# Kernel tuning notes

Measured on AMD Instinct MI355X. Metric: run time of the kernel, lower is better.

Reference implementation:

```python
import jax, jax.numpy as jnp
import numpy as np

Hh, Ww, Cc = 8, 8, 16        # observation grid h, w, channels
N = Hh * Ww                  # 64 graph nodes (one per grid cell)
B = 4096                     # batch
HEADS, COUT = 4, 32          # GAT heads, per-head output dim (concat -> 128)
HID, ADIM = 128, 6           # hidden_dim, action_dim
GAT_OUT = N * HEADS * COUT   # 8192 flattened GAT output per sample
NEG = -9e15


def _grid_adj():
    # 4-connected grid graph with self loops (make_graph's static edge structure)
    A = np.zeros((N, N), np.int32)
    for r in range(Hh):
        for c in range(Ww):
            i = r * Ww + c
            A[i, i] = 1
            for dr, dc in ((1, 0), (-1, 0), (0, 1), (0, -1)):
                rr, cc = r + dr, c + dc
                if 0 <= rr < Hh and 0 <= cc < Ww:
                    A[i, rr * Ww + cc] = 1
    return jnp.asarray(A)


def setup_inputs() -> dict:
    key = jax.random.key(0)
    ks = iter(jax.random.split(key, 40))
    p = lambda *s: jax.random.normal(next(ks), s, jnp.float32) * 0.1
    z = lambda *s: jnp.zeros(s, jnp.float32)
    return dict(
        x=jax.random.normal(next(ks), (B, Hh * Ww * Cc), jnp.float32),
        adj=_grid_adj(),
        actor_h=z(B, HID), actor_c=z(B, HID),
        critic_h=z(B, HID), critic_c=z(B, HID),
        gat1_W=p(Cc, HEADS * COUT), gat1_b=z(HEADS * COUT), gat1_a=p(HEADS, 2 * COUT),
        d1_W=p(GAT_OUT, HID), d1_b=z(HID),
        lstm1_Wi=p(HID, 4 * HID), lstm1_Wh=p(HID, 4 * HID), lstm1_b=z(4 * HID),
        ln1_s=jnp.ones((HID,), jnp.float32), ln1_bi=z(HID),
        d2_W=p(HID, HID), d2_b=z(HID),
        d3_W=p(HID, HID), d3_b=z(HID),
        dout_W=p(HID, ADIM), dout_b=z(ADIM),
        gat2_W=p(Cc, HEADS * COUT), gat2_b=z(HEADS * COUT), gat2_a=p(HEADS, 2 * COUT),
        c1_W=p(GAT_OUT, HID), c1_b=z(HID),
        lstm2_Wi=p(HID, 4 * HID), lstm2_Wh=p(HID, 4 * HID), lstm2_b=z(4 * HID),
        ln2_s=jnp.ones((HID,), jnp.float32), ln2_bi=z(HID),
        c2_W=p(HID, HID), c2_b=z(HID),
        c3_W=p(HID, HID), c3_b=z(HID),
        cout_W=p(HID, 1), cout_b=z(1),
    )


def _gat(feats, adj, W, b, a):
    # feats: [B,N,Cc]; adj: [N,N] int; multi-head GAT with concat heads
    h = (feats @ W + b).reshape(B, N, HEADS, COUT)           # [B,N,H,C]
    ls = jnp.einsum('bnhc,hc->bnh', h, a[:, :COUT])          # source logit
    ld = jnp.einsum('bnhc,hc->bnh', h, a[:, COUT:])          # dest logit
    logits = jax.nn.leaky_relu(ls[:, :, None, :] + ld[:, None, :, :], 0.2)  # [B,N,N,H]
    logits = jnp.where(adj[None, :, :, None] > 0, logits, NEG)
    attn = jax.nn.softmax(logits, axis=2)                    # over neighbors
    return jnp.einsum('bnmh,bmhc->bnhc', attn, h).reshape(B, -1)  # [B, N*H*C]


def _lstm(h, c, xin, Wi, Wh, bh):
    # flax OptimizedLSTMCell: gates in order i,f,g,o; bias only on hidden path
    z = xin @ Wi + h @ Wh + bh
    i, f, g, o = jnp.split(z, 4, axis=-1)
    nc = jax.nn.sigmoid(f) * c + jax.nn.sigmoid(i) * jnp.tanh(g)
    nh = jax.nn.sigmoid(o) * jnp.tanh(nc)
    return nh, nc


def _ln(v, s, b):
    mu = v.mean(-1, keepdims=True)
    var = v.var(-1, keepdims=True)
    return (v - mu) * jax.lax.rsqrt(var + 1e-6) * s + b


def reference(x, adj, actor_h, actor_c, critic_h, critic_c,
              gat1_W, gat1_b, gat1_a, d1_W, d1_b,
              lstm1_Wi, lstm1_Wh, lstm1_b, ln1_s, ln1_bi,
              d2_W, d2_b, d3_W, d3_b, dout_W, dout_b,
              gat2_W, gat2_b, gat2_a, c1_W, c1_b,
              lstm2_Wi, lstm2_Wh, lstm2_b, ln2_s, ln2_bi,
              c2_W, c2_b, c3_W, c3_b, cout_W, cout_b):
    act = jnp.tanh
    feats = x.reshape(B, N, Cc)
    # actor branch
    am = act(_gat(feats, adj, gat1_W, gat1_b, gat1_a) @ d1_W + d1_b)
    a_h, a_c = _lstm(actor_h, actor_c, am, lstm1_Wi, lstm1_Wh, lstm1_b)
    am = _ln(a_h, ln1_s, ln1_bi)
    am = act(am @ d2_W + d2_b)
    am = act(am @ d3_W + d3_b)
    logits = am @ dout_W + dout_b                            # Categorical logits
    # critic branch
    cm = act(_gat(feats, adj, gat2_W, gat2_b, gat2_a) @ c1_W + c1_b)
    c_h, c_c = _lstm(critic_h, critic_c, cm, lstm2_Wi, lstm2_Wh, lstm2_b)
    cm = _ln(c_h, ln2_s, ln2_bi)
    cm = act(cm @ c2_W + c2_b)
    cm = act(cm @ c3_W + c3_b)
    value = (cm @ cout_W + cout_b).squeeze(-1)
    return logits, value, a_h, a_c, c_h, c_c
```

## Files before the change

kernel.cpp:

```cpp
#include <hip/hip_runtime.h>
#include <hip/hip_bf16.h>

#define BATCH 4096
#define NN    64
#define CIN   16
#define NHEAD 4
#define CO    32
#define HC    128
#define HID   128
#define ADIM  6
#define K1    8192
#define LDH   136
#define KSPLIT 8

typedef __attribute__((ext_vector_type(8))) short bf16x8;
typedef __attribute__((ext_vector_type(8))) unsigned short u16x8;
typedef __attribute__((ext_vector_type(4))) float f32x4;

__device__ __forceinline__ float bf2f(unsigned short u) {
    unsigned int v = ((unsigned int)u) << 16;
    return __uint_as_float(v);
}
__device__ __forceinline__ unsigned short f2bf(float x) {
    union { __hip_bfloat16 h; unsigned short u; } cv;
    cv.h = __float2bfloat16(x);
    return cv.u;
}
__device__ __forceinline__ float sigmf(float x) { return 1.f / (1.f + expf(-x)); }

__device__ __forceinline__ void gload_lds16(const void* g, void* l) {
    __builtin_amdgcn_global_load_lds(
        (const __attribute__((address_space(1))) unsigned int*)(uintptr_t)g,
        (__attribute__((address_space(3))) unsigned int*)(uintptr_t)l,
        16, 0, 0);
}

struct TJob { const float* in; unsigned short* out; int K; int N; int ldo; };
struct TJobs { TJob j[8]; };

__global__ __launch_bounds__(256) void k_prep(
    const float* __restrict__ d1W, const float* __restrict__ c1W,
    unsigned short* __restrict__ Wt1, unsigned short* __restrict__ Wt2,
    TJobs jobs,
    const float* __restrict__ ha, const float* __restrict__ hc,
    unsigned short* __restrict__ X,
    const int* __restrict__ adj, unsigned long long* __restrict__ masks,
    const float* __restrict__ l1b, const float* __restrict__ l2b,
    const float* __restrict__ b2,  const float* __restrict__ c2b,
    const float* __restrict__ b3,  const float* __restrict__ c3b,
    float* __restrict__ biasz, float* __restrict__ b2p, float* __restrict__ b3p,
    const float* __restrict__ g1W, const float* __restrict__ g2W,
    const float* __restrict__ g1a, const float* __restrict__ g2a,
    const float* __restrict__ g1b, const float* __restrict__ g2b,
    unsigned short* __restrict__ wtg,
    float* __restrict__ blsld)
{
    const int bid = blockIdx.x;
    const int t   = threadIdx.x;

    if (bid < 1024) {
        __shared__ float s[64][33];
        const int  zsel = bid >> 9;
        const float* W  = zsel ? c1W : d1W;
        unsigned short* Wt = zsel ? Wt2 : Wt1;
        const int k0 = (bid & 127) * 64;
        const int n0 = ((bid >> 7) & 3) * 32;
        const int kr = t >> 5, nc = t & 31;
#pragma unroll
        for (int i = 0; i < 8; ++i)
            s[kr + 8 * i][nc] = W[(size_t)(k0 + kr + 8 * i) * HC + n0 + nc];
        __syncthreads();
#pragma unroll
        for (int j = 0; j < 8; ++j) {
            const int idx = j * 256 + t;
            const int n = idx >> 6, k = idx & 63;
            Wt[(size_t)(n0 + n) * K1 + k0 + k] = f2bf(s[k][n]);
        }
    } else if (bid < 1536) {
        const int b   = bid - 1024;
        const int job = b >> 6, idx = b & 63;
        const TJob jb = jobs.j[job];
        const int ntk = jb.K >> 5, ntn = jb.N >> 5;
        if (idx >= ntk * ntn) return;
        const int tk = idx % ntk, tn = idx / ntk;
        __shared__ float s2[32][33];
        const int kr = t >> 5, nc = t & 31;
        const int k0 = tk * 32, n0 = tn * 32;
#pragma unroll
        for (int i = 0; i < 4; ++i)
            s2[kr + 8 * i][nc] = jb.in[(size_t)(k0 + kr + 8 * i) * jb.N + n0 + nc];
        __syncthreads();
#pragma unroll
        for (int i = 0; i < 4; ++i) {
            const int idx2 = i * 256 + t;
            const int n = idx2 >> 5, k = idx2 & 31;
            jb.out[(size_t)(n0 + n) * jb.ldo + k0 + k] = f2bf(s2[k][n]);
        }
    } else if (bid < 2560) {
        const int gid = (bid - 1536) * 256 + t;
        const int zi  = gid >> 17;
        const int rem = gid & 131071;
        const int s3  = rem >> 5, c4 = rem & 31;
        const float4 v = reinterpret_cast<const float4*>(zi ? hc : ha)[(size_t)s3 * 32 + c4];
        ushort4 u;
        u.x = f2bf(v.x); u.y = f2bf(v.y); u.z = f2bf(v.z); u.w = f2bf(v.w);
        reinterpret_cast<ushort4*>(X + (size_t)zi * BATCH * 256 + (size_t)s3 * 256 + 128)[c4] = u;
    } else {
#pragma unroll
        for (int it = 0; it < 4; ++it) {
            const int tt = t + it * 256;
            if (tt < NN) {
                unsigned long long m = 0ull;
                for (int j = 0; j < NN; ++j)
                    if (adj[tt * NN + j] > 0) m |= (1ull << j);
                masks[tt] = m;
            }
            biasz[tt] = (tt < 512) ? l1b[tt] : l2b[tt - 512];
            if (tt < HID) {
                b2p[tt]       = b2[tt];
                b2p[HID + tt] = c2b[tt];
                b3p[tt]       = b3[tt];
                b3p[HID + tt] = c3b[tt];
            }
        }
#pragma unroll
        for (int q = 0; q < 16; ++q) {
            const int idx = t * 16 + q;
            const int set = idx >> 11;
            const int rem = idx & 2047;
            const int col = rem >> 4, k = rem & 15;
            wtg[set * 2304 + col * 16 + k] = f2bf((set ? g2W : g1W)[k * HC + col]);
        }
        {
            const int set = t >> 7, rem = t & 127;
            const int e = rem >> 4, k = rem & 15;
            const float* W  = set ? g2W : g1W;
            const float* aa = set ? g2a : g1a;
            const int hdh = e & 3, off = (e < 4) ? 0 : 32;
            float v = 0.f;
            for (int c = 0; c < 32; ++c)
                v += W[k * HC + hdh * 32 + c] * aa[hdh * 64 + off + c];
            wtg[set * 2304 + (128 + e) * 16 + k] = f2bf(v);
            wtg[set * 2304 + (136 + e) * 16 + k] = 0;
        }
        if (t < 16) {
            const int s2 = t >> 3, e2 = t & 7;
            const float* bb2 = s2 ? g2b : g1b;
            const float* aa2 = s2 ? g2a : g1a;
            const int h2 = e2 & 3, o2 = (e2 < 4) ? 0 : 32;
            float bv = 0.f;
            for (int c = 0; c < 32; ++c)
                bv += bb2[h2 * 32 + c] * aa2[h2 * 64 + o2 + c];
            blsld[s2 * 8 + e2] = bv;
        }
    }
}

struct GatW { const unsigned short* Wt; const float* b; const float* bls; unsigned short* out; };
struct GatArgs { GatW g[2]; };

__global__ __launch_bounds__(256) void k_gat(
    const float* __restrict__ x,
    const unsigned long long* __restrict__ masks,
    GatArgs ga, int zbase)
{
    const GatW gw = ga.g[zbase + blockIdx.y];
    const unsigned short* __restrict__ Wtg = gw.Wt;
    const float* __restrict__ bias = gw.b;
    const float* __restrict__ bls  = gw.bls;
    unsigned short* __restrict__ out = gw.out;

    union UB {
        struct { unsigned short feat[64][16]; unsigned short wt[144][16]; } stg;
        unsigned short P[2][64][72];
    };
    __shared__ UB u;
    __shared__ unsigned short s_hT[128][72];
    __shared__ float s_ls[64][4];
    __shared__ float s_ld[64][4];
    __shared__ float s_bias[HC];
    __shared__ float s_bls[8];
    __shared__ unsigned long long s_mask[NN];

    const int t = threadIdx.x;
    const int b = blockIdx.x;

    {
        const int n = t >> 2, c0 = (t & 3) * 4;
        const float4 v = reinterpret_cast<const float4*>(x + (size_t)b * (NN * CIN))[t];
        ushort4 q;
        q.x = f2bf(v.x); q.y = f2bf(v.y); q.z = f2bf(v.z); q.w = f2bf(v.w);
        *reinterpret_cast<ushort4*>(&u.stg.feat[n][c0]) = q;
        if (t < 144) {
            *reinterpret_cast<u16x8*>(&u.stg.wt[t][0]) = *reinterpret_cast<const u16x8*>(Wtg + t * 16);
            *reinterpret_cast<u16x8*>(&u.stg.wt[t][8]) = *reinterpret_cast<const u16x8*>(Wtg + t * 16 + 8);
        }
        if (t < HC) s_bias[t] = bias[t];
        if (t < 8)  s_bls[t] = bls[t];
        if (t < NN) s_mask[t] = masks[t];
    }
    __syncthreads();

    const int w = t >> 6, lane = t & 63;
    const int row16 = lane & 15;
    const int jr4   = lane >> 4;

    {
        const bool lo = lane < 32;
        const int k0 = (jr4 & 1) * 8;
        const bf16x8 zf = { 0, 0, 0, 0, 0, 0, 0, 0 };
        const bf16x8 aF = lo ? *reinterpret_cast<const bf16x8*>(&u.stg.feat[w * 16 + row16][k0]) : zf;
        bf16x8 bF[9];
#pragma unroll
        for (int ct = 0; ct < 9; ++ct)
            bF[ct] = lo ? *reinterpret_cast<const bf16x8*>(&u.stg.wt[ct * 16 + row16][k0]) : zf;
        f32x4 acc[9] = {};
#pragma unroll
        for (int ct = 0; ct < 9; ++ct)
            acc[ct] = __builtin_amdgcn_mfma_f32_16x16x32_bf16(aF, bF[ct], acc[ct], 0, 0, 0);
#pragma unroll
        for (int ct = 0; ct < 8; ++ct) {
            const int col = ct * 16 + row16;
            const float bv = s_bias[col];
            ushort4 q;
            q.x = f2bf(acc[ct][0] + bv);
            q.y = f2bf(acc[ct][1] + bv);
            q.z = f2bf(acc[ct][2] + bv);
            q.w = f2bf(acc[ct][3] + bv);
            *reinterpret_cast<ushort4*>(&s_hT[col][w * 16 + jr4 * 4]) = q;
        }
        if (row16 < 8) {
            const float bb = s_bls[row16];
#pragma unroll
            for (int j = 0; j < 4; ++j) {
                const int r = w * 16 + jr4 * 4 + j;
                if (row16 < 4) s_ls[r][row16]     = acc[8][j] + bb;
                else           s_ld[r][row16 - 4] = acc[8][j] + bb;
            }
        }
    }
    __syncthreads();

    const int n  = t >> 2;
    const int hd = t & 3;
    float p[5]; int mc[5]; bool ok[5];
    {
        const unsigned long long m = s_mask[n];
        const int cand[5] = { n - 8, n - 1, n, n + 1, n + 8 };
#pragma unroll
        for (int e = 0; e < 5; ++e) {
            const int cm = cand[e];
            const bool inr = (cm >= 0) && (cm < NN);
            mc[e] = inr ? cm : n;
            ok[e] = inr && ((m >> mc[e]) & 1ull);
        }
        const float lsn = s_ls[n][hd];
        float sum = 0.f;
#pragma unroll
        for (int e = 0; e < 5; ++e) {
            float v = lsn + s_ld[mc[e]][hd];
            v = (v > 0.f) ? v : 0.2f * v;
            p[e] = ok[e] ? __expf(v) : 0.f;
            sum += p[e];
        }
        const float inv = 1.f / sum;
#pragma unroll
        for (int e = 0; e < 5; ++e) p[e] *= inv;
    }

    {
        char* pb = (char*)&u.P[0][0][0];
#pragma unroll
        for (int i = 0; i < 9; ++i)
            *reinterpret_cast<unsigned long long*>(pb + t * 72 + i * 8) = 0ull;
    }
    __syncthreads();

    unsigned short* ob = out + (size_t)b * K1;

#pragma unroll
    for (int pass = 0; pass < 2; ++pass) {
        if ((hd >> 1) == pass) {
#pragma unroll
            for (int e = 0; e < 5; ++e)
                if (ok[e]) u.P[hd & 1][n][mc[e]] = f2bf(p[e]);
        }
        __syncthreads();

        const int hh  = pass * 2 + (w >> 1);
        const int ph  = w >> 1;
        const int mtb = (w & 1) * 2;
        f32x4 acc[2][2] = {};
#pragma unroll
        for (int kt = 0; kt < 2; ++kt) {
            const int kof = kt * 32 + jr4 * 8;
            bf16x8 aF[2], bF[2];
#pragma unroll
            for (int mtl = 0; mtl < 2; ++mtl)
                aF[mtl] = *reinterpret_cast<const bf16x8*>(&u.P[ph][(mtb + mtl) * 16 + row16][kof]);
#pragma unroll
            for (int nt = 0; nt < 2; ++nt)
                bF[nt] = *reinterpret_cast<const bf16x8*>(&s_hT[hh * 32 + nt * 16 + row16][kof]);
#pragma unroll
            for (int mtl = 0; mtl < 2; ++mtl)
#pragma unroll
                for (int nt = 0; nt < 2; ++nt)
                    acc[mtl][nt] = __builtin_amdgcn_mfma_f32_16x16x32_bf16(
                        aF[mtl], bF[nt], acc[mtl][nt], 0, 0, 0);
        }
#pragma unroll
        for (int mtl = 0; mtl < 2; ++mtl)
#pragma unroll
            for (int nt = 0; nt < 2; ++nt) {
                const int ch = hh * 32 + nt * 16 + row16;
#pragma unroll
                for (int j = 0; j < 4; ++j) {
                    const int node = (mtb + mtl) * 16 + jr4 * 4 + j;
                    ob[node * HC + ch] = f2bf(acc[mtl][nt][j]);
                }
            }
        if (pass == 0) __syncthreads();
    }
}

__global__ __launch_bounds__(256) void k_mmsk(
    const unsigned short* __restrict__ A0, const unsigned short* __restrict__ A1,
    const unsigned short* __restrict__ Bt0, const unsigned short* __restrict__ Bt1,
    float* __restrict__ accum)
{
    __shared__ unsigned short sbuf[2][160 * 64];

    const int br   = blockIdx.y;
    const unsigned short* A  = br ? A1 : A0;
    const unsigned short* Bt = br ? Bt1 : Bt0;
    float* acc_out = accum + (size_t)br * BATCH * HID;

    const int t    = threadIdx.x;
    const int w    = t >> 6;
    const int lane = t & 63;
    const int m0   = blockIdx.x * 32;
    const int kbase = blockIdx.z * (K1 / KSPLIT);
    const int kiters = (K1 / KSPLIT) / 64;

    const char* srcp[5];
    int ldsoff[5];
#pragma unroll
    for (int q = 0; q < 5; ++q) {
        const int c     = w * 5 + q;
        const int p     = c * 1024 + lane * 16;
        const int prow  = p >> 7;
        const int pslot = (p >> 4) & 7;
        const int lslot = pslot ^ (prow & 7);
        ldsoff[q] = c * 1024;
        if (c < 4)
            srcp[q] = (const char*)(A + (size_t)(m0 + prow) * K1 + kbase + lslot * 8);
        else
            srcp[q] = (const char*)(Bt + (size_t)(prow - 32) * K1 + kbase + lslot * 8);
    }

    f32x4 acc[2][2] = {};

#pragma unroll
    for (int q = 0; q < 5; ++q)
        gload_lds16(srcp[q], (char*)&sbuf[0][0] + ldsoff[q]);
    __syncthreads();

    int buf = 0;
    for (int it = 0; it < kiters; ++it) {
        if (it + 1 < kiters) {
            const size_t kbyte = (size_t)(it + 1) * 128;
#pragma unroll
            for (int q = 0; q < 5; ++q)
                gload_lds16(srcp[q] + kbyte, (char*)&sbuf[buf ^ 1][0] + ldsoff[q]);
        }
        const char* bb = (const char*)&sbuf[buf][0];
        bf16x8 aF[2][2], bF[2][2];
#pragma unroll
        for (int kb = 0; kb < 2; ++kb) {
            const int slot = kb * 4 + (lane >> 4);
#pragma unroll
            for (int rb = 0; rb < 2; ++rb) {
                const int row = rb * 16 + (lane & 15);
                aF[rb][kb] = *(const bf16x8*)(bb + row * 128 + ((slot ^ (row & 7)) << 4));
            }
#pragma unroll
            for (int cb = 0; cb < 2; ++cb) {
                const int row = 32 + w * 32 + cb * 16 + (lane & 15);
                bF[cb][kb] = *(const bf16x8*)(bb + row * 128 + ((slot ^ (row & 7)) << 4));
            }
        }
#pragma unroll
        for (int kb = 0; kb < 2; ++kb)
#pragma unroll
            for (int rb = 0; rb < 2; ++rb)
#pragma unroll
                for (int cb = 0; cb < 2; ++cb)
                    acc[rb][cb] = __builtin_amdgcn_mfma_f32_16x16x32_bf16(
                        aF[rb][kb], bF[cb][kb], acc[rb][cb], 0, 0, 0);
        __syncthreads();
        buf ^= 1;
    }

    const int col0 = w * 32;
    const int r0   = (lane >> 4) * 4;
    const int cc   = lane & 15;
#pragma unroll
    for (int rb = 0; rb < 2; ++rb)
#pragma unroll
        for (int cb = 0; cb < 2; ++cb) {
            const int col = col0 + cb * 16 + cc;
#pragma unroll
            for (int j = 0; j < 4; ++j) {
                const int row = m0 + rb * 16 + r0 + j;
                atomicAdd(&acc_out[(size_t)row * HID + col], acc[rb][cb][j]);
            }
        }
}

__global__ __launch_bounds__(256) void k_epi(
    const float* __restrict__ accum,
    const float* __restrict__ biasA, const float* __restrict__ biasB,
    unsigned short* __restrict__ X)
{
    const int zi  = blockIdx.y;
    const int gid = blockIdx.x * 256 + threadIdx.x;
    const int s = gid >> 5, c4 = gid & 31;
    const float* bias = zi ? biasB : biasA;
    const float4 v  = reinterpret_cast<const float4*>(accum + (size_t)zi * BATCH * HID)[gid];
    const float4 bv = reinterpret_cast<const float4*>(bias)[c4];
    ushort4 u;
    u.x = f2bf(tanhf(v.x + bv.x));
    u.y = f2bf(tanhf(v.y + bv.y));
    u.z = f2bf(tanhf(v.z + bv.z));
    u.w = f2bf(tanhf(v.w + bv.w));
    unsigned short* Xo = X + (size_t)zi * BATCH * 256;
    reinterpret_cast<ushort4*>(Xo + (size_t)s * 256)[c4] = u;
}

__global__ __launch_bounds__(256) void k_mm(
    const unsigned short* __restrict__ A, size_t aZ, int lda,
    const unsigned short* __restrict__ Bt, size_t bZ,
    const float* __restrict__ bias, size_t biasZ,
    float* __restrict__ outF, unsigned short* __restrict__ outB,
    size_t oZ, int ldo, int kiters, int act)
{
    __shared__ unsigned short sbuf[2][160 * 64];

    const int t    = threadIdx.x;
    const int w    = t >> 6;
    const int lane = t & 63;
    const int m0   = blockIdx.x * 32;
    const int n0   = blockIdx.y * 128;
    const int z    = blockIdx.z;
    const int K    = kiters * 64;

    const unsigned short* Az = A  + (size_t)z * aZ;
    const unsigned short* Bz = Bt + (size_t)z * bZ + (size_t)n0 * K;

    const char* srcp[5];
    int ldsoff[5];
#pragma unroll
    for (int q = 0; q < 5; ++q) {
        const int c     = w * 5 + q;
        const int p     = c * 1024 + lane * 16;
        const int prow  = p >> 7;
        const int pslot = (p >> 4) & 7;
        const int lslot = pslot ^ (prow & 7);
        ldsoff[q] = c * 1024;
        if (c < 4)
            srcp[q] = (const char*)(Az + (size_t)(m0 + prow) * lda + lslot * 8);
        else
            srcp[q] = (const char*)(Bz + (size_t)(prow - 32) * K + lslot * 8);
    }

    f32x4 acc[2][2] = {};

#pragma unroll
    for (int q = 0; q < 5; ++q)
        gload_lds16(srcp[q], (char*)&sbuf[0][0] + ldsoff[q]);
    __syncthreads();

    int buf = 0;
    for (int it = 0; it < kiters; ++it) {
        if (it + 1 < kiters) {
            const size_t kbyte = (size_t)(it + 1) * 128;
#pragma unroll
            for (int q = 0; q < 5; ++q)
                gload_lds16(srcp[q] + kbyte, (char*)&sbuf[buf ^ 1][0] + ldsoff[q]);
        }
        const char* bb = (const char*)&sbuf[buf][0];
        bf16x8 aF[2][2], bF[2][2];
#pragma unroll
        for (int kb = 0; kb < 2; ++kb) {
            const int slot = kb * 4 + (lane >> 4);
#pragma unroll
            for (int rb = 0; rb < 2; ++rb) {
                const int row = rb * 16 + (lane & 15);
                aF[rb][kb] = *(const bf16x8*)(bb + row * 128 + ((slot ^ (row & 7)) << 4));
            }
#pragma unroll
            for (int cb = 0; cb < 2; ++cb) {
                const int row = 32 + w * 32 + cb * 16 + (lane & 15);
                bF[cb][kb] = *(const bf16x8*)(bb + row * 128 + ((slot ^ (row & 7)) << 4));
            }
        }
#pragma unroll
        for (int kb = 0; kb < 2; ++kb)
#pragma unroll
            for (int rb = 0; rb < 2; ++rb)
#pragma unroll
                for (int cb = 0; cb < 2; ++cb)
                    acc[rb][cb] = __builtin_amdgcn_mfma_f32_16x16x32_bf16(
                        aF[rb][kb], bF[cb][kb], acc[rb][cb], 0, 0, 0);
        __syncthreads();
        buf ^= 1;
    }

    const int col0 = w * 32;
    const int r0   = (lane >> 4) * 4;
    const int cc   = lane & 15;
#pragma unroll
    for (int rb = 0; rb < 2; ++rb)
#pragma unroll
        for (int cb = 0; cb < 2; ++cb) {
            const int col = col0 + cb * 16 + cc;
            const float bv = bias ? bias[(size_t)z * biasZ + n0 + col] : 0.f;
#pragma unroll
            for (int j = 0; j < 4; ++j) {
                const int row = m0 + rb * 16 + r0 + j;
                float v = acc[rb][cb][j] + bv;
                if (act) v = tanhf(v);
                const size_t off = (size_t)z * oZ + (size_t)row * ldo + n0 + col;
                if (outB) outB[off] = f2bf(v);
                else      outF[off] = v;
            }
        }
}

__global__ __launch_bounds__(256) void k_tail(
    const float* __restrict__ zbuf,
    const float* __restrict__ c0a, const float* __restrict__ c0c,
    const float* __restrict__ sA,  const float* __restrict__ bA,
    const float* __restrict__ sC,  const float* __restrict__ bC,
    const unsigned short* __restrict__ W23t,
    const float* __restrict__ b2p, const float* __restrict__ b3p,
    const float* __restrict__ doW, const float* __restrict__ dob,
    const float* __restrict__ coW, const float* __restrict__ cob,
    float* __restrict__ hA, float* __restrict__ cA,
    float* __restrict__ hC, float* __restrict__ cC,
    float* __restrict__ logits, float* __restrict__ value)
{
    __shared__ unsigned short s_ln[32][LDH];
    __shared__ unsigned short s_t2[32][LDH];
    __shared__ unsigned short s_t3[32][LDH];
    __shared__ unsigned short s_w[128][LDH];

    const int t  = threadIdx.x;
    const int zi = blockIdx.y;
    const int s0 = blockIdx.x * 32;

    const unsigned short* W2 = W23t + (size_t)zi * HID * HID;
    const unsigned short* W3 = W23t + (size_t)(2 + zi) * HID * HID;

    {
        const int s  = t >> 3, l8 = t & 7;
        const int gb = s0 + s;
        const float* zr  = zbuf + (size_t)zi * BATCH * 512 + (size_t)gb * 512;
        const float* c0  = (zi ? c0c : c0a) + (size_t)gb * HID;
        float* oh = (zi ? hC : hA) + (size_t)gb * HID;
        float* oc = (zi ? cC : cA) + (size_t)gb * HID;
        const float* lns = zi ? sC : sA;
        const float* lnb = zi ? bC : bA;
        const int u0 = l8 * 16;

        float nh16[16];
        float sum = 0.f, sumsq = 0.f;
#pragma unroll
        for (int r4 = 0; r4 < 4; ++r4) {
            const int u = u0 + r4 * 4;
            const float4 gi = *reinterpret_cast<const float4*>(&zr[u]);
            const float4 gf = *reinterpret_cast<const float4*>(&zr[128 + u]);
            const float4 gg = *reinterpret_cast<const float4*>(&zr[256 + u]);
            const float4 go = *reinterpret_cast<const float4*>(&zr[384 + u]);
            const float4 cv = *reinterpret_cast<const float4*>(&c0[u]);
            float4 ncv, nhv;
            ncv.x = sigmf(gf.x) * cv.x + sigmf(gi.x) * tanhf(gg.x);
            ncv.y = sigmf(gf.y) * cv.y + sigmf(gi.y) * tanhf(gg.y);
            ncv.z = sigmf(gf.z) * cv.z + sigmf(gi.z) * tanhf(gg.z);
            ncv.w = sigmf(gf.w) * cv.w + sigmf(gi.w) * tanhf(gg.w);
            nhv.x = sigmf(go.x) * tanhf(ncv.x);
            nhv.y = sigmf(go.y) * tanhf(ncv.y);
            nhv.z = sigmf(go.z) * tanhf(ncv.z);
            nhv.w = sigmf(go.w) * tanhf(ncv.w);
            *reinterpret_cast<float4*>(&oc[u]) = ncv;
            *reinterpret_cast<float4*>(&oh[u]) = nhv;
            nh16[r4 * 4 + 0] = nhv.x; nh16[r4 * 4 + 1] = nhv.y;
            nh16[r4 * 4 + 2] = nhv.z; nh16[r4 * 4 + 3] = nhv.w;
            sum   += nhv.x + nhv.y + nhv.z + nhv.w;
            sumsq += nhv.x * nhv.x + nhv.y * nhv.y + nhv.z * nhv.z + nhv.w * nhv.w;
        }
        for (int msk = 1; msk < 8; msk <<= 1) {
            sum   += __shfl_xor(sum, msk, 8);
            sumsq += __shfl_xor(sumsq, msk, 8);
        }
        const float mu   = sum * (1.f / 128.f);
        const float var  = sumsq * (1.f / 128.f) - mu * mu;
        const float rstd = rsqrtf(var + 1e-6f);
        u16x8 lo, hi;
#pragma unroll
        for (int r = 0; r < 8; ++r) {
            lo[r] = f2bf((nh16[r] - mu) * rstd * lns[u0 + r] + lnb[u0 + r]);
            hi[r] = f2bf((nh16[8 + r] - mu) * rstd * lns[u0 + 8 + r] + lnb[u0 + 8 + r]);
        }
        *reinterpret_cast<u16x8*>(&s_ln[s][u0])     = lo;
        *reinterpret_cast<u16x8*>(&s_ln[s][u0 + 8]) = hi;

        const int col = t >> 1, half = (t & 1) * 64;
#pragma unroll
        for (int q = 0; q < 8; ++q) {
            const u16x8 wv = *reinterpret_cast<const u16x8*>(W2 + col * HID + half + q * 8);
            *reinterpret_cast<u16x8*>(&s_w[col][half + q * 8]) = wv;
        }
    }
    __syncthreads();

    const int w = t >> 6, lane = t & 63;
    const int row16 = lane & 15, k08 = (lane >> 4) * 8;

    {
        f32x4 acc[2][2] = {};
#pragma unroll
        for (int ks = 0; ks < 4; ++ks) {
            bf16x8 aF[2], bF[2];
#pragma unroll
            for (int rt = 0; rt < 2; ++rt)
                aF[rt] = *reinterpret_cast<const bf16x8*>(&s_ln[rt * 16 + row16][ks * 32 + k08]);
#pragma unroll
            for (int ct = 0; ct < 2; ++ct)
                bF[ct] = *reinterpret_cast<const bf16x8*>(&s_w[w * 32 + ct * 16 + row16][ks * 32 + k08]);
#pragma unroll
            for (int rt = 0; rt < 2; ++rt)
#pragma unroll
                for (int ct = 0; ct < 2; ++ct)
                    acc[rt][ct] = __builtin_amdgcn_mfma_f32_16x16x32_bf16(
                        aF[rt], bF[ct], acc[rt][ct], 0, 0, 0);
        }
#pragma unroll
        for (int rt = 0; rt < 2; ++rt)
#pragma unroll
            for (int ct = 0; ct < 2; ++ct) {
                const int col = w * 32 + ct * 16 + row16;
                const float bv = b2p[zi * HID + col];
#pragma unroll
                for (int j = 0; j < 4; ++j)
                    s_t2[rt * 16 + (lane >> 4) * 4 + j][col] = f2bf(tanhf(acc[rt][ct][j] + bv));
            }
    }
    __syncthreads();

    {
        const int col = t >> 1, half = (t & 1) * 64;
#pragma unroll
        for (int q = 0; q < 8; ++q) {
            const u16x8 wv = *reinterpret_cast<const u16x8*>(W3 + col * HID + half + q * 8);
            *reinterpret_cast<u16x8*>(&s_w[col][half + q * 8]) = wv;
        }
    }
    __syncthreads();

    {
        f32x4 acc[2][2] = {};
#pragma unroll
        for (int ks = 0; ks < 4; ++ks) {
            bf16x8 aF[2], bF[2];
#pragma unroll
            for (int rt = 0; rt < 2; ++rt)
                aF[rt] = *reinterpret_cast<const bf16x8*>(&s_t2[rt * 16 + row16][ks * 32 + k08]);
#pragma unroll
            for (int ct = 0; ct < 2; ++ct)
                bF[ct] = *reinterpret_cast<const bf16x8*>(&s_w[w * 32 + ct * 16 + row16][ks * 32 + k08]);
#pragma unroll
            for (int rt = 0; rt < 2; ++rt)
#pragma unroll
                for (int ct = 0; ct < 2; ++ct)
                    acc[rt][ct] = __builtin_amdgcn_mfma_f32_16x16x32_bf16(
                        aF[rt], bF[ct], acc[rt][ct], 0, 0, 0);
        }
#pragma unroll
        for (int rt = 0; rt < 2; ++rt)
#pragma unroll
            for (int ct = 0; ct < 2; ++ct) {
                const int col = w * 32 + ct * 16 + row16;
                const float bv = b3p[zi * HID + col];
#pragma unroll
                for (int j = 0; j < 4; ++j)
                    s_t3[rt * 16 + (lane >> 4) * 4 + j][col] = f2bf(tanhf(acc[rt][ct][j] + bv));
            }
    }
    __syncthreads();

    if (zi == 0) {
        if (t < 32 * ADIM) {
            const int s = t / ADIM, a2 = t % ADIM;
            float acc = dob[a2];
            for (int k = 0; k < HID; ++k)
                acc = fmaf(bf2f(s_t3[s][k]), doW[k * ADIM + a2], acc);
            logits[(size_t)(s0 + s) * ADIM + a2] = acc;
        }
    } else {
        if (t < 32) {
            float acc = cob[0];
            for (int k = 0; k < HID; ++k)
                acc = fmaf(bf2f(s_t3[t][k]), coW[k], acc);
            value[s0 + t] = acc;
        }
    }
}

extern "C" void kernel_launch(void* const* d_in, const int* in_sizes, int n_in,
                              void* d_out, int out_size, void* d_ws, size_t ws_size,
                              hipStream_t stream)
{
    (void)in_sizes; (void)n_in; (void)out_size;

    const float* x        = (const float*)d_in[0];
    const int*   adj      = (const int*)  d_in[1];
    const float* actor_h  = (const float*)d_in[2];
    const float* actor_c  = (const float*)d_in[3];
    const float* critic_h = (const float*)d_in[4];
    const float* critic_c = (const float*)d_in[5];
    const float* gat1_W   = (const float*)d_in[6];
    const float* gat1_b   = (const float*)d_in[7];
    const float* gat1_a   = (const float*)d_in[8];
    const float* d1_W     = (const float*)d_in[9];
    const float* d1_b     = (const float*)d_in[10];
    const float* l1_Wi    = (const float*)d_in[11];
    const float* l1_Wh    = (const float*)d_in[12];
    const float* l1_b     = (const float*)d_in[13];
    const float* ln1_s    = (const float*)d_in[14];
    const float* ln1_b    = (const float*)d_in[15];
    const float* d2_W     = (const float*)d_in[16];
    const float* d2_b     = (const float*)d_in[17];
    const float* d3_W     = (const float*)d_in[18];
    const float* d3_b     = (const float*)d_in[19];
    const float* dout_W   = (const float*)d_in[20];
    const float* dout_b   = (const float*)d_in[21];
    const float* gat2_W   = (const float*)d_in[22];
    const float* gat2_b   = (const float*)d_in[23];
    const float* gat2_a   = (const float*)d_in[24];
    const float* c1_W     = (const float*)d_in[25];
    const float* c1_b     = (const float*)d_in[26];
    const float* l2_Wi    = (const float*)d_in[27];
    const float* l2_Wh    = (const float*)d_in[28];
    const float* l2_b     = (const float*)d_in[29];
    const float* ln2_s    = (const float*)d_in[30];
    const float* ln2_b    = (const float*)d_in[31];
    const float* c2_W     = (const float*)d_in[32];
    const float* c2_b     = (const float*)d_in[33];
    const float* c3_W     = (const float*)d_in[34];
    const float* c3_b     = (const float*)d_in[35];
    const float* cout_W   = (const float*)d_in[36];
    const float* cout_b   = (const float*)d_in[37];

    float* out      = (float*)d_out;
    float* o_logits = out;
    float* o_value  = out + (size_t)BATCH * ADIM;
    float* o_ah     = o_value + BATCH;
    float* o_ac     = o_ah + (size_t)BATCH * HID;
    float* o_ch     = o_ac + (size_t)BATCH * HID;
    float* o_cc     = o_ch + (size_t)BATCH * HID;

    char* ws = (char*)d_ws;
    const size_t MB = 1024 * 1024;
    const size_t KB = 1024;
    unsigned long long* masks = (unsigned long long*)ws;
    float* bias_z = (float*)(ws + 4 * KB);
    float* b2p    = (float*)(ws + 8 * KB);
    float* b3p    = (float*)(ws + 12 * KB);
    unsigned short* wtg = (unsigned short*)(ws + 16 * KB);
    float* blsld  = (float*)(ws + 60 * KB);
    float* accum  = (float*)(ws + 64 * KB);
    unsigned short* Wt1  = (unsigned short*)(ws + 64 * KB + 4 * MB);
    unsigned short* Wt2  = (unsigned short*)(ws + 64 * KB + 6 * MB);
    unsigned short* Wcat = (unsigned short*)(ws + 64 * KB + 8 * MB);
    unsigned short* W23t = (unsigned short*)(ws + 64 * KB + 8 * MB + 512 * KB);
    unsigned short* X    = (unsigned short*)(ws + 64 * KB + 8 * MB + 768 * KB);
    const size_t off_big = 64 * KB + 8 * MB + 768 * KB + 4 * MB;
    char* big = ws + off_big;
    unsigned short* gatA = (unsigned short*)big;
    const bool dual = ws_size >= off_big + 128 * MB;
    unsigned short* gatB = dual ? (unsigned short*)(big + 64 * MB) : gatA;
    float*          zbuf = (float*)big;

    TJobs tj;
    tj.j[0] = { l1_Wi, Wcat,                        HID, 512, 256 };
    tj.j[1] = { l1_Wh, Wcat + 128,                  HID, 512, 256 };
    tj.j[2] = { l2_Wi, Wcat + 512 * 256,            HID, 512, 256 };
    tj.j[3] = { l2_Wh, Wcat + 512 * 256 + 128,      HID, 512, 256 };
    tj.j[4] = { d2_W,  W23t,                        HID, HID, HID };
    tj.j[5] = { c2_W,  W23t + 128 * 128,            HID, HID, HID };
    tj.j[6] = { d3_W,  W23t + 2 * 128 * 128,        HID, HID, HID };
    tj.j[7] = { c3_W,  W23t + 3 * 128 * 128,        HID, HID, HID };
    hipLaunchKernelGGL(k_prep, dim3(2561), dim3(256), 0, stream,
                       d1_W, c1_W, Wt1, Wt2, tj,
                       actor_h, critic_h, X,
                       adj, masks, l1_b, l2_b, d2_b, c2_b, d3_b, c3_b,
                       bias_z, b2p, b3p, gat1_W, gat2_W,
                       gat1_a, gat2_a, gat1_b, gat2_b, wtg, blsld);

    GatArgs ga;
    ga.g[0] = { wtg,        gat1_b, blsld,     gatA };
    ga.g[1] = { wtg + 2304, gat2_b, blsld + 8, gatB };

    if (dual) {
        hipMemsetAsync(accum, 0, (size_t)2 * BATCH * HID * 4, stream);
        hipLaunchKernelGGL(k_gat, dim3(BATCH, 2), dim3(256), 0, stream,
                           x, masks, ga, 0);
        hipLaunchKernelGGL(k_mmsk, dim3(BATCH / 32, 2, KSPLIT), dim3(256), 0, stream,
                           gatA, gatB, Wt1, Wt2, accum);
        hipLaunchKernelGGL(k_epi, dim3(512, 2), dim3(256), 0, stream,
                           accum, d1_b, c1_b, X);
    } else {
        hipLaunchKernelGGL(k_gat, dim3(BATCH, 1), dim3(256), 0, stream,
                           x, masks, ga, 0);
        hipMemsetAsync(accum, 0, (size_t)BATCH * HID * 4, stream);
        hipLaunchKernelGGL(k_mmsk, dim3(BATCH / 32, 1, KSPLIT), dim3(256), 0, stream,
                           gatA, gatA, Wt1, Wt1, accum);
        hipLaunchKernelGGL(k_epi, dim3(512, 1), dim3(256), 0, stream,
                           accum, d1_b, c1_b, X);
        hipLaunchKernelGGL(k_gat, dim3(BATCH, 1), dim3(256), 0, stream,
                           x, masks, ga, 1);
        hipMemsetAsync(accum, 0, (size_t)BATCH * HID * 4, stream);
        hipLaunchKernelGGL(k_mmsk, dim3(BATCH / 32, 1, KSPLIT), dim3(256), 0, stream,
                           gatA, gatA, Wt2, Wt2, accum);
        hipLaunchKernelGGL(k_epi, dim3(512, 1), dim3(256), 0, stream,
                           accum, c1_b, c1_b, X + (size_t)BATCH * 256);
    }

    hipLaunchKernelGGL(k_mm, dim3(BATCH / 32, 4, 2), dim3(256), 0, stream,
                       X, (size_t)BATCH * 256, 256, Wcat, (size_t)512 * 256,
                       bias_z, (size_t)512,
                       zbuf, (unsigned short*)nullptr, (size_t)BATCH * 512, 512, 4, 0);

    hipLaunchKernelGGL(k_tail, dim3(BATCH / 32, 2), dim3(256), 0, stream,
                       zbuf, actor_c, critic_c, ln1_s, ln1_b, ln2_s, ln2_b,
                       W23t, b2p, b3p, dout_W, dout_b, cout_W, cout_b,
                       o_ah, o_ac, o_ch, o_cc, o_logits, o_value);
}
```

Baseline: 133.9 us.

## Fuse LSTM gate GEMM into tail kernel, dropping separate k_mm launch

Moves the LSTM gate matmul (X times Wcat plus bias) out of the standalone k_mm kernel and into the tail kernel. Gate pre-activations go into shared memory instead of a global fp32 buffer, and shared memory is reused through a union across phases. This removes one kernel launch and the write and re-read of a 4096x512x2 fp32 intermediate. In exchange, B fragments are read straight from global/L2 without LDS staging, and each block does more serial work with lower occupancy from a larger LDS footprint.

```diff
diff --git a/kernel.cpp b/kernel.cpp
--- a/kernel.cpp
+++ b/kernel.cpp
@@ -437,108 +437,10 @@
     reinterpret_cast<ushort4*>(Xo + (size_t)s * 256)[c4] = u;
 }
 
-__global__ __launch_bounds__(256) void k_mm(
-    const unsigned short* __restrict__ A, size_t aZ, int lda,
-    const unsigned short* __restrict__ Bt, size_t bZ,
-    const float* __restrict__ bias, size_t biasZ,
-    float* __restrict__ outF, unsigned short* __restrict__ outB,
-    size_t oZ, int ldo, int kiters, int act)
-{
-    __shared__ unsigned short sbuf[2][160 * 64];
-
-    const int t    = threadIdx.x;
-    const int w    = t >> 6;
-    const int lane = t & 63;
-    const int m0   = blockIdx.x * 32;
-    const int n0   = blockIdx.y * 128;
-    const int z    = blockIdx.z;
-    const int K    = kiters * 64;
-
-    const unsigned short* Az = A  + (size_t)z * aZ;
-    const unsigned short* Bz = Bt + (size_t)z * bZ + (size_t)n0 * K;
-
-    const char* srcp[5];
-    int ldsoff[5];
-#pragma unroll
-    for (int q = 0; q < 5; ++q) {
-        const int c     = w * 5 + q;
-        const int p     = c * 1024 + lane * 16;
-        const int prow  = p >> 7;
-        const int pslot = (p >> 4) & 7;
-        const int lslot = pslot ^ (prow & 7);
-        ldsoff[q] = c * 1024;
-        if (c < 4)
-            srcp[q] = (const char*)(Az + (size_t)(m0 + prow) * lda + lslot * 8);
-        else
-            srcp[q] = (const char*)(Bz + (size_t)(prow - 32) * K + lslot * 8);
-    }
-
-    f32x4 acc[2][2] = {};
-
-#pragma unroll
-    for (int q = 0; q < 5; ++q)
-        gload_lds16(srcp[q], (char*)&sbuf[0][0] + ldsoff[q]);
-    __syncthreads();
-
-    int buf = 0;
-    for (int it = 0; it < kiters; ++it) {
-        if (it + 1 < kiters) {
-            const size_t kbyte = (size_t)(it + 1) * 128;
-#pragma unroll
-            for (int q = 0; q < 5; ++q)
-                gload_lds16(srcp[q] + kbyte, (char*)&sbuf[buf ^ 1][0] + ldsoff[q]);
-        }
-        const char* bb = (const char*)&sbuf[buf][0];
-        bf16x8 aF[2][2], bF[2][2];
-#pragma unroll
-        for (int kb = 0; kb < 2; ++kb) {
-            const int slot = kb * 4 + (lane >> 4);
-#pragma unroll
-            for (int rb = 0; rb < 2; ++rb) {
-                const int row = rb * 16 + (lane & 15);
-                aF[rb][kb] = *(const bf16x8*)(bb + row * 128 + ((slot ^ (row & 7)) << 4));
-            }
-#pragma unroll
-            for (int cb = 0; cb < 2; ++cb) {
-                const int row = 32 + w * 32 + cb * 16 + (lane & 15);
-                bF[cb][kb] = *(const bf16x8*)(bb + row * 128 + ((slot ^ (row & 7)) << 4));
-            }
-        }
-#pragma unroll
-        for (int kb = 0; kb < 2; ++kb)
-#pragma unroll
-            for (int rb = 0; rb < 2; ++rb)
-#pragma unroll
-                for (int cb = 0; cb < 2; ++cb)
-                    acc[rb][cb] = __builtin_amdgcn_mfma_f32_16x16x32_bf16(
-                        aF[rb][kb], bF[cb][kb], acc[rb][cb], 0, 0, 0);
-        __syncthreads();
-        buf ^= 1;
-    }
-
-    const int col0 = w * 32;
-    const int r0   = (lane >> 4) * 4;
-    const int cc   = lane & 15;
-#pragma unroll
-    for (int rb = 0; rb < 2; ++rb)
-#pragma unroll
-        for (int cb = 0; cb < 2; ++cb) {
-            const int col = col0 + cb * 16 + cc;
-            const float bv = bias ? bias[(size_t)z * biasZ + n0 + col] : 0.f;
-#pragma unroll
-            for (int j = 0; j < 4; ++j) {
-                const int row = m0 + rb * 16 + r0 + j;
-                float v = acc[rb][cb][j] + bv;
-                if (act) v = tanhf(v);
-                const size_t off = (size_t)z * oZ + (size_t)row * ldo + n0 + col;
-                if (outB) outB[off] = f2bf(v);
-                else      outF[off] = v;
-            }
-        }
-}
-
-__global__ __launch_bounds__(256) void k_tail(
-    const float* __restrict__ zbuf,
+__global__ __launch_bounds__(256) void k_tail2(
+    const unsigned short* __restrict__ X,
+    const unsigned short* __restrict__ Wcat,
+    const float* __restrict__ biasz,
     const float* __restrict__ c0a, const float* __restrict__ c0c,
     const float* __restrict__ sA,  const float* __restrict__ bA,
     const float* __restrict__ sC,  const float* __restrict__ bC,
@@ -550,82 +452,128 @@
     float* __restrict__ hC, float* __restrict__ cC,
     float* __restrict__ logits, float* __restrict__ value)
 {
+    union UTail {
+        struct { unsigned short Xb[32][264]; float z[16][516]; } p1;
+        struct {
+            unsigned short w[128][LDH];
+            unsigned short t2[32][LDH];
+            unsigned short t3[32][LDH];
+        } p2;
+    };
+    __shared__ UTail u;
     __shared__ unsigned short s_ln[32][LDH];
-    __shared__ unsigned short s_t2[32][LDH];
-    __shared__ unsigned short s_t3[32][LDH];
-    __shared__ unsigned short s_w[128][LDH];
 
     const int t  = threadIdx.x;
     const int zi = blockIdx.y;
     const int s0 = blockIdx.x * 32;
 
+    const unsigned short* Xz = X    + (size_t)zi * BATCH * 256;
+    const unsigned short* Wz = Wcat + (size_t)zi * 512 * 256;
     const unsigned short* W2 = W23t + (size_t)zi * HID * HID;
     const unsigned short* W3 = W23t + (size_t)(2 + zi) * HID * HID;
 
     {
-        const int s  = t >> 3, l8 = t & 7;
-        const int gb = s0 + s;
-        const float* zr  = zbuf + (size_t)zi * BATCH * 512 + (size_t)gb * 512;
-        const float* c0  = (zi ? c0c : c0a) + (size_t)gb * HID;
-        float* oh = (zi ? hC : hA) + (size_t)gb * HID;
-        float* oc = (zi ? cC : cA) + (size_t)gb * HID;
-        const float* lns = zi ? sC : sA;
-        const float* lnb = zi ? bC : bA;
-        const int u0 = l8 * 16;
-
-        float nh16[16];
-        float sum = 0.f, sumsq = 0.f;
-#pragma unroll
-        for (int r4 = 0; r4 < 4; ++r4) {
-            const int u = u0 + r4 * 4;
-            const float4 gi = *reinterpret_cast<const float4*>(&zr[u]);
-            const float4 gf = *reinterpret_cast<const float4*>(&zr[128 + u]);
-            const float4 gg = *reinterpret_cast<const float4*>(&zr[256 + u]);
-            const float4 go = *reinterpret_cast<const float4*>(&zr[384 + u]);
-            const float4 cv = *reinterpret_cast<const float4*>(&c0[u]);
-            float4 ncv, nhv;
-            ncv.x = sigmf(gf.x) * cv.x + sigmf(gi.x) * tanhf(gg.x);
-            ncv.y = sigmf(gf.y) * cv.y + sigmf(gi.y) * tanhf(gg.y);
-            ncv.z = sigmf(gf.z) * cv.z + sigmf(gi.z) * tanhf(gg.z);
-            ncv.w = sigmf(gf.w) * cv.w + sigmf(gi.w) * tanhf(gg.w);
-            nhv.x = sigmf(go.x) * tanhf(ncv.x);
-            nhv.y = sigmf(go.y) * tanhf(ncv.y);
-            nhv.z = sigmf(go.z) * tanhf(ncv.z);
-            nhv.w = sigmf(go.w) * tanhf(ncv.w);
-            *reinterpret_cast<float4*>(&oc[u]) = ncv;
-            *reinterpret_cast<float4*>(&oh[u]) = nhv;
-            nh16[r4 * 4 + 0] = nhv.x; nh16[r4 * 4 + 1] = nhv.y;
-            nh16[r4 * 4 + 2] = nhv.z; nh16[r4 * 4 + 3] = nhv.w;
-            sum   += nhv.x + nhv.y + nhv.z + nhv.w;
-            sumsq += nhv.x * nhv.x + nhv.y * nhv.y + nhv.z * nhv.z + nhv.w * nhv.w;
-        }
-        for (int msk = 1; msk < 8; msk <<= 1) {
-            sum   += __shfl_xor(sum, msk, 8);
-            sumsq += __shfl_xor(sumsq, msk, 8);
-        }
-        const float mu   = sum * (1.f / 128.f);
-        const float var  = sumsq * (1.f / 128.f) - mu * mu;
-        const float rstd = rsqrtf(var + 1e-6f);
-        u16x8 lo, hi;
-#pragma unroll
-        for (int r = 0; r < 8; ++r) {
-            lo[r] = f2bf((nh16[r] - mu) * rstd * lns[u0 + r] + lnb[u0 + r]);
-            hi[r] = f2bf((nh16[8 + r] - mu) * rstd * lns[u0 + 8 + r] + lnb[u0 + 8 + r]);
-        }
-        *reinterpret_cast<u16x8*>(&s_ln[s][u0])     = lo;
-        *reinterpret_cast<u16x8*>(&s_ln[s][u0 + 8]) = hi;
-
+        const int row = t >> 3, seg = t & 7;
+        const unsigned short* xr = Xz + (size_t)(s0 + row) * 256 + seg * 32;
+#pragma unroll
+        for (int i = 0; i < 4; ++i) {
+            const u16x8 v = *reinterpret_cast<const u16x8*>(xr + i * 8);
+            *reinterpret_cast<u16x8*>(&u.p1.Xb[row][seg * 32 + i * 8]) = v;
+        }
+    }
+    __syncthreads();
+
+    const int w = t >> 6, lane = t & 63;
+    const int row16 = lane & 15, jr4 = lane >> 4;
+    const int k08 = jr4 * 8;
+
+#pragma unroll
+    for (int half = 0; half < 2; ++half) {
+        f32x4 acc[8] = {};
+#pragma unroll
+        for (int ks = 0; ks < 8; ++ks) {
+            const int kof = ks * 32 + k08;
+            const bf16x8 aF = *reinterpret_cast<const bf16x8*>(
+                &u.p1.Xb[half * 16 + row16][kof]);
+#pragma unroll
+            for (int nt = 0; nt < 8; ++nt) {
+                const bf16x8 bF = *reinterpret_cast<const bf16x8*>(
+                    Wz + (size_t)(w * 128 + nt * 16 + row16) * 256 + kof);
+                acc[nt] = __builtin_amdgcn_mfma_f32_16x16x32_bf16(aF, bF, acc[nt], 0, 0, 0);
+            }
+        }
+#pragma unroll
+        for (int nt = 0; nt < 8; ++nt) {
+            const int unit = w * 128 + nt * 16 + row16;
+            const float bv = biasz[zi * 512 + unit];
+#pragma unroll
+            for (int j = 0; j < 4; ++j)
+                u.p1.z[jr4 * 4 + j][unit] = acc[nt][j] + bv;
+        }
+        __syncthreads();
+
+        {
+            const int s  = t >> 4, l16 = t & 15;
+            const int gb = s0 + half * 16 + s;
+            const float* zr = &u.p1.z[s][0];
+            const float* c0 = (zi ? c0c : c0a) + (size_t)gb * HID;
+            float* oh = (zi ? hC : hA) + (size_t)gb * HID;
+            float* oc = (zi ? cC : cA) + (size_t)gb * HID;
+            const float* lns = zi ? sC : sA;
+            const float* lnb = zi ? bC : bA;
+            const int u0 = l16 * 8;
+
+            float nh8[8];
+            float sum = 0.f, sumsq = 0.f;
+#pragma unroll
+            for (int r4 = 0; r4 < 2; ++r4) {
+                const int uu = u0 + r4 * 4;
+                const float4 gi = *reinterpret_cast<const float4*>(&zr[uu]);
+                const float4 gf = *reinterpret_cast<const float4*>(&zr[128 + uu]);
+                const float4 gg = *reinterpret_cast<const float4*>(&zr[256 + uu]);
+                const float4 go = *reinterpret_cast<const float4*>(&zr[384 + uu]);
+                const float4 cv = *reinterpret_cast<const float4*>(&c0[uu]);
+                float4 ncv, nhv;
+                ncv.x = sigmf(gf.x) * cv.x + sigmf(gi.x) * tanhf(gg.x);
+                ncv.y = sigmf(gf.y) * cv.y + sigmf(gi.y) * tanhf(gg.y);
+                ncv.z = sigmf(gf.z) * cv.z + sigmf(gi.z) * tanhf(gg.z);
+                ncv.w = sigmf(gf.w) * cv.w + sigmf(gi.w) * tanhf(gg.w);
+                nhv.x = sigmf(go.x) * tanhf(ncv.x);
+                nhv.y = sigmf(go.y) * tanhf(ncv.y);
+                nhv.z = sigmf(go.z) * tanhf(ncv.z);
+                nhv.w = sigmf(go.w) * tanhf(ncv.w);
+                *reinterpret_cast<float4*>(&oc[uu]) = ncv;
+                *reinterpret_cast<float4*>(&oh[uu]) = nhv;
+                nh8[r4 * 4 + 0] = nhv.x; nh8[r4 * 4 + 1] = nhv.y;
+                nh8[r4 * 4 + 2] = nhv.z; nh8[r4 * 4 + 3] = nhv.w;
+                sum   += nhv.x + nhv.y + nhv.z + nhv.w;
+                sumsq += nhv.x * nhv.x + nhv.y * nhv.y + nhv.z * nhv.z + nhv.w * nhv.w;
+            }
+            for (int msk = 1; msk < 16; msk <<= 1) {
+                sum   += __shfl_xor(sum, msk, 16);
+                sumsq += __shfl_xor(sumsq, msk, 16);
+            }
+            const float mu   = sum * (1.f / 128.f);
+            const float var  = sumsq * (1.f / 128.f) - mu * mu;
+            const float rstd = rsqrtf(var + 1e-6f);
+            u16x8 lo;
+#pragma unroll
+            for (int r = 0; r < 8; ++r)
+                lo[r] = f2bf((nh8[r] - mu) * rstd * lns[u0 + r] + lnb[u0 + r]);
+            *reinterpret_cast<u16x8*>(&s_ln[half * 16 + s][u0]) = lo;
+        }
+        __syncthreads();
+    }
+
+    {
         const int col = t >> 1, half = (t & 1) * 64;
 #pragma unroll
         for (int q = 0; q < 8; ++q) {
             const u16x8 wv = *reinterpret_cast<const u16x8*>(W2 + col * HID + half + q * 8);
-            *reinterpret_cast<u16x8*>(&s_w[col][half + q * 8]) = wv;
-        }
-    }
-    __syncthreads();
-
-    const int w = t >> 6, lane = t & 63;
-    const int row16 = lane & 15, k08 = (lane >> 4) * 8;
+            *reinterpret_cast<u16x8*>(&u.p2.w[col][half + q * 8]) = wv;
+        }
+    }
+    __syncthreads();
 
     {
         f32x4 acc[2][2] = {};
@@ -637,7 +585,7 @@
                 aF[rt] = *reinterpret_cast<const bf16x8*>(&s_ln[rt * 16 + row16][ks * 32 + k08]);
 #pragma unroll
             for (int ct = 0; ct < 2; ++ct)
-                bF[ct] = *reinterpret_cast<const bf16x8*>(&s_w[w * 32 + ct * 16 + row16][ks * 32 + k08]);
+                bF[ct] = *reinterpret_cast<const bf16x8*>(&u.p2.w[w * 32 + ct * 16 + row16][ks * 32 + k08]);
 #pragma unroll
             for (int rt = 0; rt < 2; ++rt)
 #pragma unroll
@@ -653,7 +601,7 @@
                 const float bv = b2p[zi * HID + col];
 #pragma unroll
                 for (int j = 0; j < 4; ++j)
-                    s_t2[rt * 16 + (lane >> 4) * 4 + j][col] = f2bf(tanhf(acc[rt][ct][j] + bv));
+                    u.p2.t2[rt * 16 + jr4 * 4 + j][col] = f2bf(tanhf(acc[rt][ct][j] + bv));
             }
     }
     __syncthreads();
@@ -663,7 +611,7 @@
 #pragma unroll
         for (int q = 0; q < 8; ++q) {
             const u16x8 wv = *reinterpret_cast<const u16x8*>(W3 + col * HID + half + q * 8);
-            *reinterpret_cast<u16x8*>(&s_w[col][half + q * 8]) = wv;
+            *reinterpret_cast<u16x8*>(&u.p2.w[col][half + q * 8]) = wv;
         }
     }
     __syncthreads();
@@ -675,10 +623,10 @@
             bf16x8 aF[2], bF[2];
 #pragma unroll
             for (int rt = 0; rt < 2; ++rt)
-                aF[rt] = *reinterpret_cast<const bf16x8*>(&s_t2[rt * 16 + row16][ks * 32 + k08]);
+                aF[rt] = *reinterpret_cast<const bf16x8*>(&u.p2.t2[rt * 16 + row16][ks * 32 + k08]);
 #pragma unroll
             for (int ct = 0; ct < 2; ++ct)
-                bF[ct] = *reinterpret_cast<const bf16x8*>(&s_w[w * 32 + ct * 16 + row16][ks * 32 + k08]);
+                bF[ct] = *reinterpret_cast<const bf16x8*>(&u.p2.w[w * 32 + ct * 16 + row16][ks * 32 + k08]);
 #pragma unroll
             for (int rt = 0; rt < 2; ++rt)
 #pragma unroll
@@ -694,7 +642,7 @@
                 const float bv = b3p[zi * HID + col];
 #pragma unroll
                 for (int j = 0; j < 4; ++j)
-                    s_t3[rt * 16 + (lane >> 4) * 4 + j][col] = f2bf(tanhf(acc[rt][ct][j] + bv));
+                    u.p2.t3[rt * 16 + jr4 * 4 + j][col] = f2bf(tanhf(acc[rt][ct][j] + bv));
             }
     }
     __syncthreads();
@@ -704,14 +652,14 @@
             const int s = t / ADIM, a2 = t % ADIM;
             float acc = dob[a2];
             for (int k = 0; k < HID; ++k)
-                acc = fmaf(bf2f(s_t3[s][k]), doW[k * ADIM + a2], acc);
+                acc = fmaf(bf2f(u.p2.t3[s][k]), doW[k * ADIM + a2], acc);
             logits[(size_t)(s0 + s) * ADIM + a2] = acc;
         }
     } else {
         if (t < 32) {
             float acc = cob[0];
             for (int k = 0; k < HID; ++k)
-                acc = fmaf(bf2f(s_t3[t][k]), coW[k], acc);
+                acc = fmaf(bf2f(u.p2.t3[t][k]), coW[k], acc);
             value[s0 + t] = acc;
         }
     }
@@ -790,7 +738,6 @@
     unsigned short* gatA = (unsigned short*)big;
     const bool dual = ws_size >= off_big + 128 * MB;
     unsigned short* gatB = dual ? (unsigned short*)(big + 64 * MB) : gatA;
-    float*          zbuf = (float*)big;
 
     TJobs tj;
     tj.j[0] = { l1_Wi, Wcat,                        HID, 512, 256 };
@@ -837,13 +784,9 @@
                            accum, c1_b, c1_b, X + (size_t)BATCH * 256);
     }
 
-    hipLaunchKernelGGL(k_mm, dim3(BATCH / 32, 4, 2), dim3(256), 0, stream,
-                       X, (size_t)BATCH * 256, 256, Wcat, (size_t)512 * 256,
-                       bias_z, (size_t)512,
-                       zbuf, (unsigned short*)nullptr, (size_t)BATCH * 512, 512, 4, 0);
-
-    hipLaunchKernelGGL(k_tail, dim3(BATCH / 32, 2), dim3(256), 0, stream,
-                       zbuf, actor_c, critic_c, ln1_s, ln1_b, ln2_s, ln2_b,
+    hipLaunchKernelGGL(k_tail2, dim3(BATCH / 32, 2), dim3(256), 0, stream,
+                       X, Wcat, bias_z, actor_c, critic_c,
+                       ln1_s, ln1_b, ln2_s, ln2_b,
                        W23t, b2p, b3p, dout_W, dout_b, cout_W, cout_b,
                        o_ah, o_ac, o_ch, o_cc, o_logits, o_value);
 }
```

Result: slower. 139.1 us (+3.9%).
